# Kernel tuning notes

Hardware: AMD Instinct MI355X
Metric: run time of the kernel (lower is better)

## Reference

```python
import jax, jax.numpy as jnp
import numpy as np


def setup_inputs() -> dict:
    key = jax.random.key(0)
    ks = jax.random.split(key, 7)
    B, S, D, HD, m = 4, 8192, 2048, 128, 4
    s = 0.02
    return {
        "h": jax.random.normal(ks[0], (B, S, D), jnp.float32),
        "w_kv_a": jax.random.normal(ks[1], (D, HD), jnp.float32) * s,
        "w_kv_b": jax.random.normal(ks[2], (D, HD), jnp.float32) * s,
        "w_z_a": jax.random.normal(ks[3], (D, HD), jnp.float32) * s,
        "w_z_b": jax.random.normal(ks[4], (D, HD), jnp.float32) * s,
        "b_a": jax.random.normal(ks[5], (m, HD), jnp.float32) * s,
        "b_b": jax.random.normal(ks[6], (m, HD), jnp.float32) * s,
        "m": m,
    }


def reference(h, w_kv_a, w_kv_b, w_z_a, w_z_b, b_a, b_b, m):
    # h: [B, S, D]; weights stored as [D, head_dim] (torch Linear W^T)
    B, S, D = h.shape
    HD = w_kv_a.shape[1]
    n = S // m  # number of compressed blocks
    # Projections, reshaped into m-token blocks: [B, n, m, HD]
    c_a = (h @ w_kv_a).reshape(B, n, m, HD)
    c_b = (h @ w_kv_b).reshape(B, n, m, HD)
    z_a = (h @ w_z_a).reshape(B, n, m, HD)
    z_b = (h @ w_z_b).reshape(B, n, m, HD)

    def prev(x):  # previous block per position (block 0 has no predecessor)
        return jnp.concatenate([jnp.zeros_like(x[:, :1]), x[:, :-1]], axis=1)

    # Window of 2m logits per block: [prev-block b-branch, current-block a-branch]
    logits = jnp.concatenate([prev(z_b) + b_b, z_a + b_a], axis=2)  # [B, n, 2m, HD]
    # Block 0 only sees its own m tokens: mask out the (absent) previous half
    valid = jnp.concatenate(
        [jnp.broadcast_to((jnp.arange(n) > 0)[:, None], (n, m)),
         jnp.ones((n, m), bool)], axis=1)  # [n, 2m]
    neg = jnp.finfo(logits.dtype).min
    logits = jnp.where(valid[None, :, :, None], logits, neg)
    weights = jax.nn.softmax(logits, axis=2)  # softmax over the 2m window, per feature
    c_vals = jnp.concatenate([prev(c_b), c_a], axis=2)  # [B, n, 2m, HD]
    compressed = jnp.sum(weights * c_vals, axis=2)  # [B, n, HD]
    return compressed, compressed
```

## Files before the change

kernel.cpp:

```cpp
#include <hip/hip_runtime.h>

typedef unsigned short u16;
typedef unsigned int u32;
typedef float f32x4 __attribute__((ext_vector_type(4)));
typedef short bf16x8 __attribute__((ext_vector_type(8)));
typedef u16 u16x8 __attribute__((ext_vector_type(8)));

#define D_DIM 2048
#define HD_DIM 128
#define BM 128
#define HALO 16
#define MROWS 144
#define BK 32
#define KSTEPS 64
#define NTHREADS 512
#define OUT1 1048576

#define A_STRIDE 40
#define A_BYTES (MROWS * A_STRIDE * 2)
#define B_BYTES (512 * BK * 2)
#define OFF_A (3 * B_BYTES)
#define EPI_STRIDE 520
#define SMEM_BYTES (MROWS * EPI_STRIDE * 2)

__device__ __forceinline__ u16 f2bf(float f) {
  u32 u = __builtin_bit_cast(u32, f);
  u32 r = u + 0x7FFFu + ((u >> 16) & 1u);
  return (u16)(r >> 16);
}
__device__ __forceinline__ float bf2f(u16 v) {
  u32 u = ((u32)v) << 16;
  return __builtin_bit_cast(float, u);
}

__device__ __forceinline__ void gload_lds16(const u16* g, u16* l) {
  __builtin_amdgcn_global_load_lds(
      (const __attribute__((address_space(1))) unsigned int*)g,
      (__attribute__((address_space(3))) unsigned int*)l, 16, 0, 0);
}

__global__ __launch_bounds__(256) void wconv_kernel(
    const float* __restrict__ w0, const float* __restrict__ w1,
    const float* __restrict__ w2, const float* __restrict__ w3,
    u16* __restrict__ Wt) {
  __shared__ float tile[64][129];
  const int t = threadIdx.x;
  const int mat = blockIdx.x >> 5;
  const int k0 = (blockIdx.x & 31) << 6;
  const float* w = (mat == 0) ? w0 : (mat == 1) ? w1 : (mat == 2) ? w2 : w3;
#pragma unroll
  for (int i = 0; i < 32; ++i) {
    int idx = t + i * 256;
    int r = idx >> 7, c = idx & 127;
    tile[r][c] = w[(k0 + r) * HD_DIM + c];
  }
  __syncthreads();
#pragma unroll
  for (int i = 0; i < 32; ++i) {
    int idx = t + i * 256;
    int nl = idx >> 6, kk = idx & 63;
    int n = mat * HD_DIM + nl;
    int k = k0 + kk;
    int stepi = k >> 5, kr = k & 31;
    int pos = stepi * 16384 + n * 32 + (((kr >> 3) ^ ((n >> 1) & 3)) << 3) + (kr & 7);
    Wt[pos] = f2bf(tile[kk][nl]);
  }
}

__global__ __launch_bounds__(NTHREADS, 2) void fused_kernel(
    const float* __restrict__ h, const u16* __restrict__ Wt,
    const float* __restrict__ ba, const float* __restrict__ bb,
    float* __restrict__ out) {
  __shared__ alignas(16) unsigned char smem[SMEM_BYTES];
  const int t = threadIdx.x;
  const int w = t >> 6;
  const int l = t & 63;
  const int r0 = blockIdx.x * BM;

  const int arow0 = t >> 2, aseg0 = t & 3;
  const int ag0 = r0 - HALO + arow0;
  const bool av0 = (ag0 >= 0);
  const long ag0c = av0 ? (long)ag0 : 0l;
  const float* asrc0 = h + ag0c * D_DIM + aseg0 * 8;
  const int adst0 = arow0 * A_STRIDE + aseg0 * 8;
  const bool has2 = ((t & 7) == 0);
  const int arow1 = 128 + (t >> 5);
  const int aseg1 = (t >> 3) & 3;
  const float* asrc1 = h + (long)(r0 - HALO + arow1) * D_DIM + aseg1 * 8;
  const int adst1 = arow1 * A_STRIDE + aseg1 * 8;

  const int aoff0 = (l & 15) * A_STRIDE + (l >> 4) * 8;
  const int swzr = (l >> 4) ^ ((l >> 1) & 3);
  const int boff0 = (w * 64 + (l & 15)) * 32 + swzr * 8;

  f32x4 acc[9][4];
#pragma unroll
  for (int mt = 0; mt < 9; ++mt)
#pragma unroll
    for (int nt = 0; nt < 4; ++nt) acc[mt][nt] = (f32x4){0.f, 0.f, 0.f, 0.f};

  float4 r0a, r0b, r0ha, r0hb, r1a, r1b, r1ha, r1hb;

#define ISSUE_B(SI, BI)                                           \
  {                                                               \
    const u16* gsrc = Wt + (size_t)(SI) * 16384 + w * 2048 + l * 8; \
    u16* lb = (u16*)(smem + (BI) * B_BYTES) + w * 2048;           \
    gload_lds16(gsrc, lb);                                        \
    gload_lds16(gsrc + 512, lb + 512);                            \
    gload_lds16(gsrc + 1024, lb + 1024);                          \
    gload_lds16(gsrc + 1536, lb + 1536);                          \
  }

#define ISSUE_A(SI, RA, RB, RHA, RHB)      \
  {                                        \
    const float* p0 = asrc0 + (SI) * BK;   \
    RA = *(const float4*)(p0);             \
    RB = *(const float4*)(p0 + 4);         \
    if (has2) {                            \
      const float* p1 = asrc1 + (SI) * BK; \
      RHA = *(const float4*)(p1);          \
      RHB = *(const float4*)(p1 + 4);      \
    }                                      \
  }

#define WRITE_A(BI, RA, RB, RHA, RHB)                  \
  {                                                    \
    u16* Ab = (u16*)(smem + OFF_A + (BI) * A_BYTES);   \
    u16x8 pa;                                          \
    pa[0] = av0 ? f2bf(RA.x) : (u16)0;                 \
    pa[1] = av0 ? f2bf(RA.y) : (u16)0;                 \
    pa[2] = av0 ? f2bf(RA.z) : (u16)0;                 \
    pa[3] = av0 ? f2bf(RA.w) : (u16)0;                 \
    pa[4] = av0 ? f2bf(RB.x) : (u16)0;                 \
    pa[5] = av0 ? f2bf(RB.y) : (u16)0;                 \
    pa[6] = av0 ? f2bf(RB.z) : (u16)0;                 \
    pa[7] = av0 ? f2bf(RB.w) : (u16)0;                 \
    *(u16x8*)(Ab + adst0) = pa;                        \
    if (has2) {                                        \
      u16x8 pb;                                        \
      pb[0] = f2bf(RHA.x); pb[1] = f2bf(RHA.y);        \
      pb[2] = f2bf(RHA.z); pb[3] = f2bf(RHA.w);        \
      pb[4] = f2bf(RHB.x); pb[5] = f2bf(RHB.y);        \
      pb[6] = f2bf(RHB.z); pb[7] = f2bf(RHB.w);        \
      *(u16x8*)(Ab + adst1) = pb;                      \
    }                                                  \
  }

#define COMPUTE(BI)                                                         \
  {                                                                         \
    const u16* Ab = (const u16*)(smem + OFF_A + (BI) * A_BYTES);            \
    const u16* Bb = (const u16*)(smem + (BI) * B_BYTES);                    \
    bf16x8 bfr0 = *(const bf16x8*)(Bb + boff0);                             \
    bf16x8 bfr1 = *(const bf16x8*)(Bb + boff0 + 512);                       \
    bf16x8 bfr2 = *(const bf16x8*)(Bb + boff0 + 1024);                      \
    bf16x8 bfr3 = *(const bf16x8*)(Bb + boff0 + 1536);                      \
    _Pragma("unroll")                                                       \
    for (int mt = 0; mt < 9; ++mt) {                                        \
      bf16x8 af = *(const bf16x8*)(Ab + aoff0 + mt * (16 * A_STRIDE));      \
      acc[mt][0] = __builtin_amdgcn_mfma_f32_16x16x32_bf16(af, bfr0, acc[mt][0], 0, 0, 0); \
      acc[mt][1] = __builtin_amdgcn_mfma_f32_16x16x32_bf16(af, bfr1, acc[mt][1], 0, 0, 0); \
      acc[mt][2] = __builtin_amdgcn_mfma_f32_16x16x32_bf16(af, bfr2, acc[mt][2], 0, 0, 0); \
      acc[mt][3] = __builtin_amdgcn_mfma_f32_16x16x32_bf16(af, bfr3, acc[mt][3], 0, 0, 0); \
    }                                                                       \
  }

#define VM_WAIT8() asm volatile("s_waitcnt vmcnt(8)" ::: "memory")
#define VM_WAIT0() asm volatile("s_waitcnt vmcnt(0)" ::: "memory")
#define SYNC_ITER()                                        \
  {                                                        \
    asm volatile("s_waitcnt lgkmcnt(0)" ::: "memory");     \
    __builtin_amdgcn_s_barrier();                          \
  }

  ISSUE_B(0, 0)
  ISSUE_A(0, r0a, r0b, r0ha, r0hb)
  ISSUE_B(1, 1)
  ISSUE_A(1, r1a, r1b, r1ha, r1hb)
  VM_WAIT8();
  WRITE_A(0, r0a, r0b, r0ha, r0hb)
  SYNC_ITER();

  for (int s = 0; s < KSTEPS - 2; s += 2) {
    const int b0 = s % 3, b1 = (s + 1) % 3, b2 = (s + 2) % 3, b3 = (s + 3) % 3;
    ISSUE_B(s + 2, b2)
    ISSUE_A(s + 2, r0a, r0b, r0ha, r0hb)
    VM_WAIT8();
    WRITE_A(b1, r1a, r1b, r1ha, r1hb)
    COMPUTE(b0)
    SYNC_ITER();
    ISSUE_B(s + 3, b3)
    ISSUE_A(s + 3, r1a, r1b, r1ha, r1hb)
    VM_WAIT8();
    WRITE_A(b2, r0a, r0b, r0ha, r0hb)
    COMPUTE(b1)
    SYNC_ITER();
  }
  VM_WAIT0();
  WRITE_A(0, r1a, r1b, r1ha, r1hb)
  COMPUTE(2)
  SYNC_ITER();
  COMPUTE(0)
  __syncthreads();

  u16* E = (u16*)smem;
  {
    const int er = (l >> 4) * 4;
    const int ec = w * 64 + (l & 15);
#pragma unroll
    for (int mt = 0; mt < 9; ++mt)
#pragma unroll
      for (int nt = 0; nt < 4; ++nt)
#pragma unroll
        for (int j = 0; j < 4; ++j)
          E[(mt * 16 + er + j) * EPI_STRIDE + ec + nt * 16] =
              f2bf(acc[mt][nt][j]);
  }
  __syncthreads();

  {
    const int hd = t & 127;
    const int grp = t >> 7;
    const int b = r0 >> 13;
    const int sbase = r0 & 8191;
#pragma unroll
    for (int i = 0; i < 8; ++i) {
      const int nblk = grp * 8 + i;
      const int s_in = sbase + nblk * 4;
      const bool first = (s_in == 0);
      const int rc = HALO + nblk * 4;
      float la[4], lb[4], ca[4], cb[4];
#pragma unroll
      for (int j = 0; j < 4; ++j) {
        const u16* rowc = E + (rc + j) * EPI_STRIDE;
        const u16* rowp = E + (rc - 4 + j) * EPI_STRIDE;
        la[j] = bf2f(rowc[256 + hd]) + ba[j * 128 + hd];
        ca[j] = bf2f(rowc[hd]);
        lb[j] = first ? -3.0e38f : (bf2f(rowp[384 + hd]) + bb[j * 128 + hd]);
        cb[j] = bf2f(rowp[128 + hd]);
      }
      float mx = la[0];
#pragma unroll
      for (int j = 1; j < 4; ++j) mx = fmaxf(mx, la[j]);
#pragma unroll
      for (int j = 0; j < 4; ++j) mx = fmaxf(mx, lb[j]);
      float num = 0.f, den = 0.f;
#pragma unroll
      for (int j = 0; j < 4; ++j) {
        float ea = __expf(la[j] - mx);
        num += ea * ca[j]; den += ea;
        float eb = __expf(lb[j] - mx);
        num += eb * cb[j]; den += eb;
      }
      const float res = num / den;
      const int o = ((b << 11) + (s_in >> 2)) * HD_DIM + hd;
      out[o] = res;
      out[o + OUT1] = res;
    }
  }
}

extern "C" void kernel_launch(void* const* d_in, const int* in_sizes, int n_in,
                              void* d_out, int out_size, void* d_ws,
                              size_t ws_size, hipStream_t stream) {
  (void)in_sizes; (void)n_in; (void)out_size; (void)ws_size;
  const float* h = (const float*)d_in[0];
  const float* w_kv_a = (const float*)d_in[1];
  const float* w_kv_b = (const float*)d_in[2];
  const float* w_z_a = (const float*)d_in[3];
  const float* w_z_b = (const float*)d_in[4];
  const float* b_a = (const float*)d_in[5];
  const float* b_b = (const float*)d_in[6];
  u16* Wt = (u16*)d_ws;
  float* out = (float*)d_out;
  wconv_kernel<<<128, 256, 0, stream>>>(w_kv_a, w_kv_b, w_z_a, w_z_b, Wt);
  fused_kernel<<<256, NTHREADS, 0, stream>>>(h, Wt, b_a, b_b, out);
}
```

Before: 421.5 us.

## Load weight fragments directly to registers and run epilogue from accumulators

```diff
diff --git a/kernel.cpp b/kernel.cpp
--- a/kernel.cpp
+++ b/kernel.cpp
@@ -18,25 +18,12 @@
 
 #define A_STRIDE 40
 #define A_BYTES (MROWS * A_STRIDE * 2)
-#define B_BYTES (512 * BK * 2)
-#define OFF_A (3 * B_BYTES)
-#define EPI_STRIDE 520
-#define SMEM_BYTES (MROWS * EPI_STRIDE * 2)
+#define SMEM_BYTES (2 * A_BYTES)
 
 __device__ __forceinline__ u16 f2bf(float f) {
   u32 u = __builtin_bit_cast(u32, f);
   u32 r = u + 0x7FFFu + ((u >> 16) & 1u);
   return (u16)(r >> 16);
-}
-__device__ __forceinline__ float bf2f(u16 v) {
-  u32 u = ((u32)v) << 16;
-  return __builtin_bit_cast(float, u);
-}
-
-__device__ __forceinline__ void gload_lds16(const u16* g, u16* l) {
-  __builtin_amdgcn_global_load_lds(
-      (const __attribute__((address_space(1))) unsigned int*)g,
-      (__attribute__((address_space(3))) unsigned int*)l, 16, 0, 0);
 }
 
 __global__ __launch_bounds__(256) void wconv_kernel(
@@ -61,9 +48,8 @@
     int nl = idx >> 6, kk = idx & 63;
     int n = mat * HD_DIM + nl;
     int k = k0 + kk;
-    int stepi = k >> 5, kr = k & 31;
-    int pos = stepi * 16384 + n * 32 + (((kr >> 3) ^ ((n >> 1) & 3)) << 3) + (kr & 7);
-    Wt[pos] = f2bf(tile[kk][nl]);
+    int s = k >> 5, slot = (k >> 3) & 3, off = k & 7;
+    Wt[(size_t)((s * 4 + slot) * 512 + n) * 8 + off] = f2bf(tile[kk][nl]);
   }
 }
 
@@ -90,25 +76,24 @@
   const int adst1 = arow1 * A_STRIDE + aseg1 * 8;
 
   const int aoff0 = (l & 15) * A_STRIDE + (l >> 4) * 8;
-  const int swzr = (l >> 4) ^ ((l >> 1) & 3);
-  const int boff0 = (w * 64 + (l & 15)) * 32 + swzr * 8;
+  const int lb_base = ((l >> 4) * 512 + w * 16 + (l & 15)) * 8;
 
   f32x4 acc[9][4];
 #pragma unroll
   for (int mt = 0; mt < 9; ++mt)
 #pragma unroll
-    for (int nt = 0; nt < 4; ++nt) acc[mt][nt] = (f32x4){0.f, 0.f, 0.f, 0.f};
+    for (int p = 0; p < 4; ++p) acc[mt][p] = (f32x4){0.f, 0.f, 0.f, 0.f};
 
   float4 r0a, r0b, r0ha, r0hb, r1a, r1b, r1ha, r1hb;
-
-#define ISSUE_B(SI, BI)                                           \
-  {                                                               \
-    const u16* gsrc = Wt + (size_t)(SI) * 16384 + w * 2048 + l * 8; \
-    u16* lb = (u16*)(smem + (BI) * B_BYTES) + w * 2048;           \
-    gload_lds16(gsrc, lb);                                        \
-    gload_lds16(gsrc + 512, lb + 512);                            \
-    gload_lds16(gsrc + 1024, lb + 1024);                          \
-    gload_lds16(gsrc + 1536, lb + 1536);                          \
+  bf16x8 B0[4], B1[4];
+
+#define ISSUE_B(SI, BARR)                                  \
+  {                                                        \
+    const u16* gp = Wt + (size_t)(SI) * 16384 + lb_base;   \
+    BARR[0] = *(const bf16x8*)(gp);                        \
+    BARR[1] = *(const bf16x8*)(gp + 1024);                 \
+    BARR[2] = *(const bf16x8*)(gp + 2048);                 \
+    BARR[3] = *(const bf16x8*)(gp + 3072);                 \
   }
 
 #define ISSUE_A(SI, RA, RB, RHA, RHB)      \
@@ -123,120 +108,100 @@
     }                                      \
   }
 
-#define WRITE_A(BI, RA, RB, RHA, RHB)                  \
-  {                                                    \
-    u16* Ab = (u16*)(smem + OFF_A + (BI) * A_BYTES);   \
-    u16x8 pa;                                          \
-    pa[0] = av0 ? f2bf(RA.x) : (u16)0;                 \
-    pa[1] = av0 ? f2bf(RA.y) : (u16)0;                 \
-    pa[2] = av0 ? f2bf(RA.z) : (u16)0;                 \
-    pa[3] = av0 ? f2bf(RA.w) : (u16)0;                 \
-    pa[4] = av0 ? f2bf(RB.x) : (u16)0;                 \
-    pa[5] = av0 ? f2bf(RB.y) : (u16)0;                 \
-    pa[6] = av0 ? f2bf(RB.z) : (u16)0;                 \
-    pa[7] = av0 ? f2bf(RB.w) : (u16)0;                 \
-    *(u16x8*)(Ab + adst0) = pa;                        \
-    if (has2) {                                        \
-      u16x8 pb;                                        \
-      pb[0] = f2bf(RHA.x); pb[1] = f2bf(RHA.y);        \
-      pb[2] = f2bf(RHA.z); pb[3] = f2bf(RHA.w);        \
-      pb[4] = f2bf(RHB.x); pb[5] = f2bf(RHB.y);        \
-      pb[6] = f2bf(RHB.z); pb[7] = f2bf(RHB.w);        \
-      *(u16x8*)(Ab + adst1) = pb;                      \
-    }                                                  \
-  }
-
-#define COMPUTE(BI)                                                         \
+#define WRITE_A(BI, RA, RB, RHA, RHB)            \
+  {                                              \
+    u16* Ab = (u16*)(smem + (BI) * A_BYTES);     \
+    u16x8 pa;                                    \
+    pa[0] = av0 ? f2bf(RA.x) : (u16)0;           \
+    pa[1] = av0 ? f2bf(RA.y) : (u16)0;           \
+    pa[2] = av0 ? f2bf(RA.z) : (u16)0;           \
+    pa[3] = av0 ? f2bf(RA.w) : (u16)0;           \
+    pa[4] = av0 ? f2bf(RB.x) : (u16)0;           \
+    pa[5] = av0 ? f2bf(RB.y) : (u16)0;           \
+    pa[6] = av0 ? f2bf(RB.z) : (u16)0;           \
+    pa[7] = av0 ? f2bf(RB.w) : (u16)0;           \
+    *(u16x8*)(Ab + adst0) = pa;                  \
+    if (has2) {                                  \
+      u16x8 pb;                                  \
+      pb[0] = f2bf(RHA.x); pb[1] = f2bf(RHA.y);  \
+      pb[2] = f2bf(RHA.z); pb[3] = f2bf(RHA.w);  \
+      pb[4] = f2bf(RHB.x); pb[5] = f2bf(RHB.y);  \
+      pb[6] = f2bf(RHB.z); pb[7] = f2bf(RHB.w);  \
+      *(u16x8*)(Ab + adst1) = pb;                \
+    }                                            \
+  }
+
+#define COMPUTE(BI, BARR)                                                   \
   {                                                                         \
-    const u16* Ab = (const u16*)(smem + OFF_A + (BI) * A_BYTES);            \
-    const u16* Bb = (const u16*)(smem + (BI) * B_BYTES);                    \
-    bf16x8 bfr0 = *(const bf16x8*)(Bb + boff0);                             \
-    bf16x8 bfr1 = *(const bf16x8*)(Bb + boff0 + 512);                       \
-    bf16x8 bfr2 = *(const bf16x8*)(Bb + boff0 + 1024);                      \
-    bf16x8 bfr3 = *(const bf16x8*)(Bb + boff0 + 1536);                      \
+    const u16* Ab = (const u16*)(smem + (BI) * A_BYTES);                    \
     _Pragma("unroll")                                                       \
     for (int mt = 0; mt < 9; ++mt) {                                        \
       bf16x8 af = *(const bf16x8*)(Ab + aoff0 + mt * (16 * A_STRIDE));      \
-      acc[mt][0] = __builtin_amdgcn_mfma_f32_16x16x32_bf16(af, bfr0, acc[mt][0], 0, 0, 0); \
-      acc[mt][1] = __builtin_amdgcn_mfma_f32_16x16x32_bf16(af, bfr1, acc[mt][1], 0, 0, 0); \
-      acc[mt][2] = __builtin_amdgcn_mfma_f32_16x16x32_bf16(af, bfr2, acc[mt][2], 0, 0, 0); \
-      acc[mt][3] = __builtin_amdgcn_mfma_f32_16x16x32_bf16(af, bfr3, acc[mt][3], 0, 0, 0); \
+      acc[mt][0] = __builtin_amdgcn_mfma_f32_16x16x32_bf16(af, BARR[0], acc[mt][0], 0, 0, 0); \
+      acc[mt][1] = __builtin_amdgcn_mfma_f32_16x16x32_bf16(af, BARR[1], acc[mt][1], 0, 0, 0); \
+      acc[mt][2] = __builtin_amdgcn_mfma_f32_16x16x32_bf16(af, BARR[2], acc[mt][2], 0, 0, 0); \
+      acc[mt][3] = __builtin_amdgcn_mfma_f32_16x16x32_bf16(af, BARR[3], acc[mt][3], 0, 0, 0); \
     }                                                                       \
   }
 
-#define VM_WAIT8() asm volatile("s_waitcnt vmcnt(8)" ::: "memory")
-#define VM_WAIT0() asm volatile("s_waitcnt vmcnt(0)" ::: "memory")
-#define SYNC_ITER()                                        \
-  {                                                        \
-    asm volatile("s_waitcnt lgkmcnt(0)" ::: "memory");     \
-    __builtin_amdgcn_s_barrier();                          \
-  }
-
-  ISSUE_B(0, 0)
+#define SYNC_ITER()                                    \
+  {                                                    \
+    asm volatile("s_waitcnt lgkmcnt(0)" ::: "memory"); \
+    __builtin_amdgcn_s_barrier();                      \
+  }
+
   ISSUE_A(0, r0a, r0b, r0ha, r0hb)
-  ISSUE_B(1, 1)
+  ISSUE_B(0, B0)
   ISSUE_A(1, r1a, r1b, r1ha, r1hb)
-  VM_WAIT8();
   WRITE_A(0, r0a, r0b, r0ha, r0hb)
   SYNC_ITER();
 
   for (int s = 0; s < KSTEPS - 2; s += 2) {
-    const int b0 = s % 3, b1 = (s + 1) % 3, b2 = (s + 2) % 3, b3 = (s + 3) % 3;
-    ISSUE_B(s + 2, b2)
+    ISSUE_B(s + 1, B1)
     ISSUE_A(s + 2, r0a, r0b, r0ha, r0hb)
-    VM_WAIT8();
-    WRITE_A(b1, r1a, r1b, r1ha, r1hb)
-    COMPUTE(b0)
+    COMPUTE(s & 1, B0)
+    WRITE_A((s + 1) & 1, r1a, r1b, r1ha, r1hb)
     SYNC_ITER();
-    ISSUE_B(s + 3, b3)
+    ISSUE_B(s + 2, B0)
     ISSUE_A(s + 3, r1a, r1b, r1ha, r1hb)
-    VM_WAIT8();
-    WRITE_A(b2, r0a, r0b, r0ha, r0hb)
-    COMPUTE(b1)
+    COMPUTE((s + 1) & 1, B1)
+    WRITE_A(s & 1, r0a, r0b, r0ha, r0hb)
     SYNC_ITER();
   }
-  VM_WAIT0();
-  WRITE_A(0, r1a, r1b, r1ha, r1hb)
-  COMPUTE(2)
+  ISSUE_B(63, B1)
+  COMPUTE(0, B0)
+  WRITE_A(1, r1a, r1b, r1ha, r1hb)
   SYNC_ITER();
-  COMPUTE(0)
-  __syncthreads();
-
-  u16* E = (u16*)smem;
+  COMPUTE(1, B1)
+
   {
-    const int er = (l >> 4) * 4;
-    const int ec = w * 64 + (l & 15);
-#pragma unroll
-    for (int mt = 0; mt < 9; ++mt)
-#pragma unroll
-      for (int nt = 0; nt < 4; ++nt)
-#pragma unroll
-        for (int j = 0; j < 4; ++j)
-          E[(mt * 16 + er + j) * EPI_STRIDE + ec + nt * 16] =
-              f2bf(acc[mt][nt][j]);
-  }
-  __syncthreads();
-
-  {
-    const int hd = t & 127;
-    const int grp = t >> 7;
+    const int g = l >> 4;
+    const int hd = (w << 4) + (l & 15);
+    const int src = (l + 48) & 63;
+    float ba_r[4], bb_r[4];
+#pragma unroll
+    for (int j = 0; j < 4; ++j) {
+      ba_r[j] = ba[j * HD_DIM + hd];
+      bb_r[j] = bb[j * HD_DIM + hd];
+    }
     const int b = r0 >> 13;
     const int sbase = r0 & 8191;
-#pragma unroll
-    for (int i = 0; i < 8; ++i) {
-      const int nblk = grp * 8 + i;
-      const int s_in = sbase + nblk * 4;
-      const bool first = (s_in == 0);
-      const int rc = HALO + nblk * 4;
+    const bool firstBlk = (sbase == 0);
+#pragma unroll
+    for (int mt = 1; mt <= 8; ++mt) {
+      const bool mask0 = firstBlk && (mt == 1) && (g == 0);
       float la[4], lb[4], ca[4], cb[4];
 #pragma unroll
       for (int j = 0; j < 4; ++j) {
-        const u16* rowc = E + (rc + j) * EPI_STRIDE;
-        const u16* rowp = E + (rc - 4 + j) * EPI_STRIDE;
-        la[j] = bf2f(rowc[256 + hd]) + ba[j * 128 + hd];
-        ca[j] = bf2f(rowc[hd]);
-        lb[j] = first ? -3.0e38f : (bf2f(rowp[384 + hd]) + bb[j * 128 + hd]);
-        cb[j] = bf2f(rowp[128 + hd]);
+        la[j] = acc[mt][2][j] + ba_r[j];
+        ca[j] = acc[mt][0][j];
+        float zb_s = __shfl(acc[mt][3][j], src, 64);
+        float zb_p = __shfl(acc[mt - 1][3][j], src, 64);
+        float cb_s = __shfl(acc[mt][1][j], src, 64);
+        float cb_p = __shfl(acc[mt - 1][1][j], src, 64);
+        float zb = (g == 0) ? zb_p : zb_s;
+        cb[j] = (g == 0) ? cb_p : cb_s;
+        lb[j] = mask0 ? -3.0e38f : (zb + bb_r[j]);
       }
       float mx = la[0];
 #pragma unroll
@@ -252,7 +217,8 @@
         num += eb * cb[j]; den += eb;
       }
       const float res = num / den;
-      const int o = ((b << 11) + (s_in >> 2)) * HD_DIM + hd;
+      const int nblk = (sbase >> 2) + (mt - 1) * 4 + g;
+      const int o = ((b << 11) + nblk) * HD_DIM + hd;
       out[o] = res;
       out[o + OUT1] = res;
     }
```

Result: faster. 405.5 us (-3.8%).
